# Kernel optimization log

Measured on AMD Instinct MI355X. Metric: run time of the kernel, lower is better.

The kernel has to match this reference:

```python
import jax, jax.numpy as jnp
import numpy as np

B, T, D = 4, 8192, 1024
C = 8.0


def setup_inputs() -> dict:
    key = jax.random.key(0)
    k1, k2, k3 = jax.random.split(key, 3)
    init_std = D ** (-0.5)
    x = jax.random.normal(k1, (B, T, D), dtype=jnp.float32)
    W_in = jax.random.truncated_normal(k2, -3.0, 3.0, (D, D), dtype=jnp.float32) * init_std
    W_gate = jax.random.truncated_normal(k3, -3.0, 3.0, (D, D), dtype=jnp.float32) * init_std
    b_in = jnp.zeros((D,), dtype=jnp.float32)
    b_gate = jnp.zeros((D,), dtype=jnp.float32)
    forget_lambda = jnp.linspace(-4.323, -9.0, D, dtype=jnp.float32)
    return {"x": x, "W_in": W_in, "b_in": b_in, "W_gate": W_gate,
            "b_gate": b_gate, "forget_lambda": forget_lambda}


def _combine(c1, c2):
    # linear recurrence h_t = a_t * h_{t-1} + b_t  (associative composition)
    a1, b1 = c1
    a2, b2 = c2
    return a1 * a2, a2 * b1 + b2


def reference(x, W_in, b_in, W_gate, b_gate, forget_lambda):
    # x: [B, T, D]
    input_gate = x @ W_in.T + b_in          # [B, T, D]
    recurrence_gate = x @ W_gate.T + b_gate  # [B, T, D]
    alpha = jnp.exp(-C * jax.nn.softplus(forget_lambda) * jax.nn.sigmoid(recurrence_gate))
    beta = jnp.sqrt(1.0 - alpha ** 2 + 1e-6)
    xbeta = beta * jax.nn.sigmoid(input_gate) * x
    # parallel scan of h_t = alpha_t * h_{t-1} + xbeta_t along sequence axis
    _, h = jax.lax.associative_scan(_combine, (alpha, xbeta), axis=1)
    return h
```

## Files before the change

kernel.cpp:

```cpp
#include <hip/hip_runtime.h>

typedef unsigned short u16;
typedef __attribute__((ext_vector_type(8))) short short8;
typedef __attribute__((ext_vector_type(4))) float f32x4;

#define T_SEQ 8192
#define DDIM 1024
#define BB 4
#define MM (BB * T_SEQ)
#define NC 128
#define CHUNK (T_SEQ / NC)
#define CHAINS (BB * DDIM)
#define NT 16

__device__ __forceinline__ float bf_lo(unsigned p) {
    union { unsigned u; float f; } v; v.u = p << 16; return v.f;
}
__device__ __forceinline__ float bf_hi(unsigned p) {
    union { unsigned u; float f; } v; v.u = p & 0xffff0000u; return v.f;
}
__device__ __forceinline__ float bf_u16(u16 p) {
    union { unsigned u; float f; } v; v.u = ((unsigned)p) << 16; return v.f;
}
__device__ __forceinline__ u16 f2bf(float f) {
    union { unsigned u; float f; } v; v.f = f;
    unsigned r = v.u + 0x7fffu + ((v.u >> 16) & 1u);
    return (u16)(r >> 16);
}
__device__ __forceinline__ float sigm(float z) {
    return __builtin_amdgcn_rcpf(1.0f + __expf(-z));
}
__device__ __forceinline__ void gld16(const u16* g, u16* l) {
    __builtin_amdgcn_global_load_lds((const __attribute__((address_space(1))) void*)g,
                                     (__attribute__((address_space(3))) void*)l, 16, 0, 0);
}

#define N4X (MM * DDIM / 4)
#define N4W (DDIM * DDIM / 4)
__global__ __launch_bounds__(256) void cvt_all(const float* __restrict__ x,
                                               const float* __restrict__ Wi,
                                               const float* __restrict__ Wg,
                                               u16* __restrict__ Xb,
                                               u16* __restrict__ Wib,
                                               u16* __restrict__ Wgb) {
    int i = blockIdx.x * 256 + threadIdx.x;
    const float* src; u16* dst; int j;
    if (i < N4X)            { src = x;  dst = Xb;  j = i; }
    else if (i < N4X + N4W) { src = Wi; dst = Wib; j = i - N4X; }
    else                    { src = Wg; dst = Wgb; j = i - N4X - N4W; }
    float4 v = ((const float4*)src)[j];
    ushort4 o;
    o.x = f2bf(v.x); o.y = f2bf(v.y); o.z = f2bf(v.z); o.w = f2bf(v.w);
    ((ushort4*)dst)[j] = o;
}


#define MFMA_ROW(i_, av)                                                              \
    acc[i_][0] = __builtin_amdgcn_mfma_f32_16x16x32_bf16(av, b0, acc[i_][0], 0, 0, 0); \
    acc[i_][1] = __builtin_amdgcn_mfma_f32_16x16x32_bf16(av, b1, acc[i_][1], 0, 0, 0); \
    acc[i_][2] = __builtin_amdgcn_mfma_f32_16x16x32_bf16(av, b2, acc[i_][2], 0, 0, 0); \
    acc[i_][3] = __builtin_amdgcn_mfma_f32_16x16x32_bf16(av, b3, acc[i_][3], 0, 0, 0);

#define MFMA_Q(ib) MFMA_ROW((ib)+0, a0) MFMA_ROW((ib)+1, a1) MFMA_ROW((ib)+2, a2) MFMA_ROW((ib)+3, a3)

#define PH_TAIL(IB)                                          \
    __builtin_amdgcn_s_barrier();                            \
    asm volatile("s_waitcnt lgkmcnt(0)" ::: "memory");       \
    __builtin_amdgcn_sched_barrier(0);                       \
    __builtin_amdgcn_s_setprio(1);                           \
    MFMA_Q(IB)                                               \
    __builtin_amdgcn_s_setprio(0);                           \
    __builtin_amdgcn_s_barrier();                            \
    __builtin_amdgcn_sched_barrier(0);

#define STA(buf, kh, rb, t_) gld16(gA + (size_t)(t_)*64 + (kh)*32 + (size_t)(rb)*128*DDIM, \
                                   &lds[(((buf)*2 + (kh))*1024 + (rb)*512 + tid)*8])
#define STB(buf, kh, hf, t_) gld16(((hf) ? gBg : gBi) + (size_t)(t_)*64 + (kh)*32,          \
                                   &lds[32768 + (((buf)*2 + (kh))*1024 + (hf)*512 + tid)*8])

#define LDA(kk, i) (*(const short8*)&lds[((cur*2 + (kk))*256 + arow0 + (i)*16)*32 + aoff])
#define LDB(kk, j) (*(const short8*)&lds[32768 + ((cur*2 + (kk))*256 + brow0 + (j)*16)*32 + aoff])

__global__ __launch_bounds__(512, 2)
void gemm_fused(const u16* __restrict__ X, const u16* __restrict__ Wi,
                const u16* __restrict__ Wg, const float* __restrict__ b_in,
                const float* __restrict__ b_gate, const float* __restrict__ lam,
                u16* __restrict__ Sg, u16* __restrict__ XBg) {
    const int bid = blockIdx.x;
    const int xcd = bid & 7;
    const int r = bid >> 3;
    const int n_tile = r & 7;
    const int m_tile = xcd * 16 + (r >> 3);
    const int tN0 = n_tile * 128;
    const int tM0 = m_tile * 256;

    const int tid = threadIdx.x;
    const int lane = tid & 63;
    const int w = tid >> 6;
    const int wm = w >> 2;
    const int wn = w & 3;
    const int gate = wn >> 1;
    const int wn_sub = wn & 1;

    __shared__ u16 lds[65536];

    const int srow = tid >> 2;
    const int c8log = (tid & 3) ^ ((tid >> 3) & 3);
    const u16* gA  = X  + (size_t)(tM0 + srow) * DDIM + c8log * 8;
    const u16* gBi = Wi + (size_t)(tN0 + srow) * DDIM + c8log * 8;
    const u16* gBg = Wg + (size_t)(tN0 + srow) * DDIM + c8log * 8;

    const int lm = lane & 15;
    const int aoff = (((lane >> 4) ^ ((lm >> 1) & 3))) * 8;
    const int arow0 = wm * 128 + lm;
    const int brow0 = gate * 128 + wn_sub * 64 + lm;

    f32x4 acc[8][4] = {};
    short8 a0, a1, a2, a3, b0, b1, b2, b3;

    STA(0, 0, 0, 0); STA(0, 0, 1, 0); STB(0, 0, 0, 0); STB(0, 0, 1, 0);
    STA(0, 1, 0, 0); STA(0, 1, 1, 0); STB(0, 1, 0, 0); STB(0, 1, 1, 0);
    asm volatile("s_waitcnt vmcnt(4)" ::: "memory");
    __builtin_amdgcn_s_barrier();
    __builtin_amdgcn_sched_barrier(0);

    for (int t = 0; t < NT - 1; ++t) {
        const int cur = t & 1, nb = cur ^ 1, tn = t + 1;
        b0 = LDB(0, 0); b1 = LDB(0, 1); b2 = LDB(0, 2); b3 = LDB(0, 3);
        a0 = LDA(0, 0); a1 = LDA(0, 1); a2 = LDA(0, 2); a3 = LDA(0, 3);
        STA(nb, 0, 0, tn); STA(nb, 0, 1, tn);
        PH_TAIL(0)
        a0 = LDA(0, 4); a1 = LDA(0, 5); a2 = LDA(0, 6); a3 = LDA(0, 7);
        STB(nb, 0, 0, tn); STB(nb, 0, 1, tn);
        asm volatile("s_waitcnt vmcnt(4)" ::: "memory");
        PH_TAIL(4)
        b0 = LDB(1, 0); b1 = LDB(1, 1); b2 = LDB(1, 2); b3 = LDB(1, 3);
        a0 = LDA(1, 0); a1 = LDA(1, 1); a2 = LDA(1, 2); a3 = LDA(1, 3);
        STA(nb, 1, 0, tn); STA(nb, 1, 1, tn);
        PH_TAIL(0)
        a0 = LDA(1, 4); a1 = LDA(1, 5); a2 = LDA(1, 6); a3 = LDA(1, 7);
        STB(nb, 1, 0, tn); STB(nb, 1, 1, tn);
        asm volatile("s_waitcnt vmcnt(4)" ::: "memory");
        PH_TAIL(4)
    }
    {
        const int cur = (NT - 1) & 1;
        b0 = LDB(0, 0); b1 = LDB(0, 1); b2 = LDB(0, 2); b3 = LDB(0, 3);
        a0 = LDA(0, 0); a1 = LDA(0, 1); a2 = LDA(0, 2); a3 = LDA(0, 3);
        PH_TAIL(0)
        a0 = LDA(0, 4); a1 = LDA(0, 5); a2 = LDA(0, 6); a3 = LDA(0, 7);
        asm volatile("s_waitcnt vmcnt(0)" ::: "memory");
        PH_TAIL(4)
        b0 = LDB(1, 0); b1 = LDB(1, 1); b2 = LDB(1, 2); b3 = LDB(1, 3);
        a0 = LDA(1, 0); a1 = LDA(1, 1); a2 = LDA(1, 2); a3 = LDA(1, 3);
        PH_TAIL(0)
        a0 = LDA(1, 4); a1 = LDA(1, 5); a2 = LDA(1, 6); a3 = LDA(1, 7);
        PH_TAIL(4)
    }

    const int pair = wm * 2 + wn_sub;
    const int r0 = (lane >> 4) << 2;
    const int cb = lane & 15;
    if (gate) {
#pragma unroll
        for (int j = 0; j < 4; ++j) {
            const int colg = tN0 + wn_sub * 64 + j * 16 + cb;
            const float bj = b_gate[colg];
            const float nsp = -8.0f * log1pf(__expf(lam[colg]));
#pragma unroll
            for (int i = 0; i < 8; ++i) {
                const int rowb = tM0 + wm * 128 + i * 16 + r0;
#pragma unroll
                for (int rr = 0; rr < 4; ++rr) {
                    float s = nsp * sigm(acc[i][j][rr] + bj);
                    u16 sb = f2bf(s);
                    Sg[(size_t)(rowb + rr) * DDIM + colg] = sb;
                    lds[((pair * 8 + i) * 16 + j * 4 + rr) * 64 + lane] = sb;
                }
            }
        }
    }
    asm volatile("s_waitcnt lgkmcnt(0)" ::: "memory");
    __builtin_amdgcn_s_barrier();
    __builtin_amdgcn_sched_barrier(0);
    if (!gate) {
#pragma unroll
        for (int j = 0; j < 4; ++j) {
            const int colg = tN0 + wn_sub * 64 + j * 16 + cb;
            const float bj = b_in[colg];
#pragma unroll
            for (int i = 0; i < 8; ++i) {
                const int rowb = tM0 + wm * 128 + i * 16 + r0;
#pragma unroll
                for (int rr = 0; rr < 4; ++rr) {
                    float s = bf_u16(lds[((pair * 8 + i) * 16 + j * 4 + rr) * 64 + lane]);
                    float a2v = __expf(2.0f * s);
                    float be = sqrtf(1.0f - a2v + 1e-6f);
                    float p = sigm(acc[i][j][rr] + bj);
                    float xv = bf_u16(X[(size_t)(rowb + rr) * DDIM + colg]);
                    XBg[(size_t)(rowb + rr) * DDIM + colg] = f2bf(be * p * xv);
                }
            }
        }
    }
}

__global__ __launch_bounds__(256)
void scan_pass1(const u16* __restrict__ S, const u16* __restrict__ XB,
                float* __restrict__ AggA, float* __restrict__ AggB) {
    const int c = blockIdx.x, dblk = blockIdx.y, bq = blockIdx.z;
    const int d0 = dblk * 512 + threadIdx.x * 2;
    size_t base = ((size_t)(bq * T_SEQ + c * CHUNK)) * DDIM + d0;

    float A0 = 1.0f, B0 = 0.0f, A1 = 1.0f, B1 = 0.0f;
#pragma unroll 8
    for (int t = 0; t < CHUNK; t++) {
        unsigned sp = *(const unsigned*)(S + base);
        unsigned xp = *(const unsigned*)(XB + base);
        float a0 = __expf(bf_lo(sp));
        float a1 = __expf(bf_hi(sp));
        B0 = fmaf(a0, B0, bf_lo(xp)); A0 *= a0;
        B1 = fmaf(a1, B1, bf_hi(xp)); A1 *= a1;
        base += DDIM;
    }
    const int chain = bq * DDIM + d0;
    float2 av; av.x = A0; av.y = A1;
    float2 bv; bv.x = B0; bv.y = B1;
    *(float2*)(AggA + (size_t)c * CHAINS + chain) = av;
    *(float2*)(AggB + (size_t)c * CHAINS + chain) = bv;
}

__global__ __launch_bounds__(256)
void scan_pass2(const float* __restrict__ AggA, const float* __restrict__ AggB,
                float* __restrict__ H0) {
    const int chain = blockIdx.x * 256 + threadIdx.x;
    float p = 0.0f;
#pragma unroll 8
    for (int c = 0; c < NC; c++) {
        H0[(size_t)c * CHAINS + chain] = p;
        p = AggA[(size_t)c * CHAINS + chain] * p + AggB[(size_t)c * CHAINS + chain];
    }
}

__global__ __launch_bounds__(256)
void scan_pass3(const u16* __restrict__ S, const u16* __restrict__ XB,
                const float* __restrict__ H0, float* __restrict__ out) {
    const int c = blockIdx.x, dblk = blockIdx.y, bq = blockIdx.z;
    const int d0 = dblk * 512 + threadIdx.x * 2;
    size_t base = ((size_t)(bq * T_SEQ + c * CHUNK)) * DDIM + d0;
    const int chain = bq * DDIM + d0;

    float2 h = *(const float2*)(H0 + (size_t)c * CHAINS + chain);
#pragma unroll 8
    for (int t = 0; t < CHUNK; t++) {
        unsigned sp = *(const unsigned*)(S + base);
        unsigned xp = *(const unsigned*)(XB + base);
        float a0 = __expf(bf_lo(sp));
        float a1 = __expf(bf_hi(sp));
        h.x = fmaf(a0, h.x, bf_lo(xp));
        h.y = fmaf(a1, h.y, bf_hi(xp));
        *(float2*)(out + base) = h;
        base += DDIM;
    }
}

extern "C" void kernel_launch(void* const* d_in, const int* in_sizes, int n_in,
                              void* d_out, int out_size, void* d_ws, size_t ws_size,
                              hipStream_t stream) {
    const float* x   = (const float*)d_in[0];
    const float* Win = (const float*)d_in[1];
    const float* bin = (const float*)d_in[2];
    const float* Wg  = (const float*)d_in[3];
    const float* bg  = (const float*)d_in[4];
    const float* lam = (const float*)d_in[5];
    float* out = (float*)d_out;

    char* w = (char*)d_ws;
    u16* Wi_bf  = (u16*)(w);
    u16* Wg_bf  = (u16*)(w + (size_t)(2) * 1024 * 1024);
    u16* Sg     = (u16*)(w + (size_t)(4) * 1024 * 1024);
    u16* XBg    = (u16*)(w + (size_t)(68) * 1024 * 1024);
    float* AggA = (float*)(w + (size_t)(132) * 1024 * 1024);
    float* AggB = (float*)(w + (size_t)(134) * 1024 * 1024);
    float* H0   = (float*)(w + (size_t)(136) * 1024 * 1024);

    u16* Xbf = (u16*)d_out;

    cvt_all<<<dim3((N4X + 2 * N4W) / 256), dim3(256), 0, stream>>>(
        x, Win, Wg, Xbf, Wi_bf, Wg_bf);

    gemm_fused<<<dim3((DDIM / 128) * (MM / 256)), dim3(512), 0, stream>>>(
        Xbf, Wi_bf, Wg_bf, bin, bg, lam, Sg, XBg);

    scan_pass1<<<dim3(NC, 2, BB), dim3(256), 0, stream>>>(Sg, XBg, AggA, AggB);
    scan_pass2<<<dim3(CHAINS / 256), dim3(256), 0, stream>>>(AggA, AggB, H0);
    scan_pass3<<<dim3(NC, 2, BB), dim3(256), 0, stream>>>(Sg, XBg, H0, out);
}
```

Before: 521.1 us.

## Stage gate epilogue through swizzled LDS for vectorized stores; merge MFMA phases

The GEMM epilogue now writes both the recurrence-gate term and the quantized input-gate sigmoid into XOR-swizzled LDS tiles. All threads then do 16-byte vectorized reads of X and 16-byte stores of S and XB, replacing scattered 2-byte global stores and loads. The main loop also goes from four half-phases with split LDS reads to two full phases: all A/B fragments are read, then 32 MFMAs run between barriers. This raises register pressure, and storing the sigmoid as 16-bit fixed point changes precision slightly.

Result: faster. 477.4 us (-8.4%).

```diff
diff --git a/kernel.cpp b/kernel.cpp
--- a/kernel.cpp
+++ b/kernel.cpp
@@ -55,23 +55,19 @@
 }
 
 
-#define MFMA_ROW(i_, av)                                                              \
+#define MROW(i_, av)                                                                   \
     acc[i_][0] = __builtin_amdgcn_mfma_f32_16x16x32_bf16(av, b0, acc[i_][0], 0, 0, 0); \
     acc[i_][1] = __builtin_amdgcn_mfma_f32_16x16x32_bf16(av, b1, acc[i_][1], 0, 0, 0); \
     acc[i_][2] = __builtin_amdgcn_mfma_f32_16x16x32_bf16(av, b2, acc[i_][2], 0, 0, 0); \
     acc[i_][3] = __builtin_amdgcn_mfma_f32_16x16x32_bf16(av, b3, acc[i_][3], 0, 0, 0);
 
-#define MFMA_Q(ib) MFMA_ROW((ib)+0, a0) MFMA_ROW((ib)+1, a1) MFMA_ROW((ib)+2, a2) MFMA_ROW((ib)+3, a3)
-
-#define PH_TAIL(IB)                                          \
-    __builtin_amdgcn_s_barrier();                            \
-    asm volatile("s_waitcnt lgkmcnt(0)" ::: "memory");       \
-    __builtin_amdgcn_sched_barrier(0);                       \
-    __builtin_amdgcn_s_setprio(1);                           \
-    MFMA_Q(IB)                                               \
-    __builtin_amdgcn_s_setprio(0);                           \
-    __builtin_amdgcn_s_barrier();                            \
-    __builtin_amdgcn_sched_barrier(0);
+#define MALL MROW(0, a0) MROW(1, a1) MROW(2, a2) MROW(3, a3) \
+             MROW(4, a4) MROW(5, a5) MROW(6, a6) MROW(7, a7)
+
+#define RDALL(kk)                                                            \
+    b0 = LDB(kk, 0); b1 = LDB(kk, 1); b2 = LDB(kk, 2); b3 = LDB(kk, 3);      \
+    a0 = LDA(kk, 0); a1 = LDA(kk, 1); a2 = LDA(kk, 2); a3 = LDA(kk, 3);      \
+    a4 = LDA(kk, 4); a5 = LDA(kk, 5); a6 = LDA(kk, 6); a7 = LDA(kk, 7);
 
 #define STA(buf, kh, rb, t_) gld16(gA + (size_t)(t_)*64 + (kh)*32 + (size_t)(rb)*128*DDIM, \
                                    &lds[(((buf)*2 + (kh))*1024 + (rb)*512 + tid)*8])
@@ -116,92 +112,112 @@
     const int brow0 = gate * 128 + wn_sub * 64 + lm;
 
     f32x4 acc[8][4] = {};
-    short8 a0, a1, a2, a3, b0, b1, b2, b3;
+    short8 a0, a1, a2, a3, a4, a5, a6, a7, b0, b1, b2, b3;
 
     STA(0, 0, 0, 0); STA(0, 0, 1, 0); STB(0, 0, 0, 0); STB(0, 0, 1, 0);
     STA(0, 1, 0, 0); STA(0, 1, 1, 0); STB(0, 1, 0, 0); STB(0, 1, 1, 0);
     asm volatile("s_waitcnt vmcnt(4)" ::: "memory");
     __builtin_amdgcn_s_barrier();
-    __builtin_amdgcn_sched_barrier(0);
 
     for (int t = 0; t < NT - 1; ++t) {
         const int cur = t & 1, nb = cur ^ 1, tn = t + 1;
-        b0 = LDB(0, 0); b1 = LDB(0, 1); b2 = LDB(0, 2); b3 = LDB(0, 3);
-        a0 = LDA(0, 0); a1 = LDA(0, 1); a2 = LDA(0, 2); a3 = LDA(0, 3);
-        STA(nb, 0, 0, tn); STA(nb, 0, 1, tn);
-        PH_TAIL(0)
-        a0 = LDA(0, 4); a1 = LDA(0, 5); a2 = LDA(0, 6); a3 = LDA(0, 7);
-        STB(nb, 0, 0, tn); STB(nb, 0, 1, tn);
+        RDALL(0)
+        STA(nb, 0, 0, tn); STA(nb, 0, 1, tn); STB(nb, 0, 0, tn); STB(nb, 0, 1, tn);
         asm volatile("s_waitcnt vmcnt(4)" ::: "memory");
-        PH_TAIL(4)
-        b0 = LDB(1, 0); b1 = LDB(1, 1); b2 = LDB(1, 2); b3 = LDB(1, 3);
-        a0 = LDA(1, 0); a1 = LDA(1, 1); a2 = LDA(1, 2); a3 = LDA(1, 3);
-        STA(nb, 1, 0, tn); STA(nb, 1, 1, tn);
-        PH_TAIL(0)
-        a0 = LDA(1, 4); a1 = LDA(1, 5); a2 = LDA(1, 6); a3 = LDA(1, 7);
-        STB(nb, 1, 0, tn); STB(nb, 1, 1, tn);
+        __builtin_amdgcn_s_barrier();
+        __builtin_amdgcn_s_setprio(1);
+        MALL
+        __builtin_amdgcn_s_setprio(0);
+        __builtin_amdgcn_s_barrier();
+        RDALL(1)
+        STA(nb, 1, 0, tn); STA(nb, 1, 1, tn); STB(nb, 1, 0, tn); STB(nb, 1, 1, tn);
         asm volatile("s_waitcnt vmcnt(4)" ::: "memory");
-        PH_TAIL(4)
+        __builtin_amdgcn_s_barrier();
+        __builtin_amdgcn_s_setprio(1);
+        MALL
+        __builtin_amdgcn_s_setprio(0);
+        __builtin_amdgcn_s_barrier();
     }
     {
         const int cur = (NT - 1) & 1;
-        b0 = LDB(0, 0); b1 = LDB(0, 1); b2 = LDB(0, 2); b3 = LDB(0, 3);
-        a0 = LDA(0, 0); a1 = LDA(0, 1); a2 = LDA(0, 2); a3 = LDA(0, 3);
-        PH_TAIL(0)
-        a0 = LDA(0, 4); a1 = LDA(0, 5); a2 = LDA(0, 6); a3 = LDA(0, 7);
+        RDALL(0)
         asm volatile("s_waitcnt vmcnt(0)" ::: "memory");
-        PH_TAIL(4)
-        b0 = LDB(1, 0); b1 = LDB(1, 1); b2 = LDB(1, 2); b3 = LDB(1, 3);
-        a0 = LDA(1, 0); a1 = LDA(1, 1); a2 = LDA(1, 2); a3 = LDA(1, 3);
-        PH_TAIL(0)
-        a0 = LDA(1, 4); a1 = LDA(1, 5); a2 = LDA(1, 6); a3 = LDA(1, 7);
-        PH_TAIL(4)
-    }
-
-    const int pair = wm * 2 + wn_sub;
+        __builtin_amdgcn_s_barrier();
+        __builtin_amdgcn_s_setprio(1);
+        MALL
+        __builtin_amdgcn_s_setprio(0);
+        __builtin_amdgcn_s_barrier();
+        RDALL(1)
+        __builtin_amdgcn_s_setprio(1);
+        MALL
+        __builtin_amdgcn_s_setprio(0);
+        __builtin_amdgcn_s_barrier();
+    }
+
     const int r0 = (lane >> 4) << 2;
     const int cb = lane & 15;
     if (gate) {
 #pragma unroll
         for (int j = 0; j < 4; ++j) {
             const int colg = tN0 + wn_sub * 64 + j * 16 + cb;
+            const int cl = wn_sub * 64 + j * 16 + cb;
             const float bj = b_gate[colg];
             const float nsp = -8.0f * log1pf(__expf(lam[colg]));
 #pragma unroll
             for (int i = 0; i < 8; ++i) {
-                const int rowb = tM0 + wm * 128 + i * 16 + r0;
+                const int rl0 = wm * 128 + i * 16 + r0;
 #pragma unroll
                 for (int rr = 0; rr < 4; ++rr) {
+                    const int rl = rl0 + rr;
                     float s = nsp * sigm(acc[i][j][rr] + bj);
-                    u16 sb = f2bf(s);
-                    Sg[(size_t)(rowb + rr) * DDIM + colg] = sb;
-                    lds[((pair * 8 + i) * 16 + j * 4 + rr) * 64 + lane] = sb;
+                    lds[rl * 128 + (cl ^ (((rl >> 2) & 7) << 4))] = f2bf(s);
                 }
             }
         }
+    } else {
+#pragma unroll
+        for (int j = 0; j < 4; ++j) {
+            const int colg = tN0 + wn_sub * 64 + j * 16 + cb;
+            const int cl = wn_sub * 64 + j * 16 + cb;
+            const float bj = b_in[colg];
+#pragma unroll
+            for (int i = 0; i < 8; ++i) {
+                const int rl0 = wm * 128 + i * 16 + r0;
+#pragma unroll
+                for (int rr = 0; rr < 4; ++rr) {
+                    const int rl = rl0 + rr;
+                    float p = sigm(acc[i][j][rr] + bj);
+                    lds[32768 + rl * 128 + (cl ^ (((rl >> 2) & 7) << 4))] =
+                        (u16)(p * 65535.0f + 0.5f);
+                }
+            }
+        }
     }
     asm volatile("s_waitcnt lgkmcnt(0)" ::: "memory");
     __builtin_amdgcn_s_barrier();
     __builtin_amdgcn_sched_barrier(0);
-    if (!gate) {
-#pragma unroll
-        for (int j = 0; j < 4; ++j) {
-            const int colg = tN0 + wn_sub * 64 + j * 16 + cb;
-            const float bj = b_in[colg];
-#pragma unroll
-            for (int i = 0; i < 8; ++i) {
-                const int rowb = tM0 + wm * 128 + i * 16 + r0;
-#pragma unroll
-                for (int rr = 0; rr < 4; ++rr) {
-                    float s = bf_u16(lds[((pair * 8 + i) * 16 + j * 4 + rr) * 64 + lane]);
-                    float a2v = __expf(2.0f * s);
-                    float be = sqrtf(1.0f - a2v + 1e-6f);
-                    float p = sigm(acc[i][j][rr] + bj);
-                    float xv = bf_u16(X[(size_t)(rowb + rr) * DDIM + colg]);
-                    XBg[(size_t)(rowb + rr) * DDIM + colg] = f2bf(be * p * xv);
-                }
-            }
+
+    const int cc = tid & 15;
+    const int rg0 = (tid >> 4) * 8;
+#pragma unroll
+    for (int k = 0; k < 8; ++k) {
+        const int rl = rg0 + k;
+        const int ch = (cc ^ (((rl >> 2) & 7) << 1)) * 8;
+        short8 sv = *(const short8*)&lds[rl * 128 + ch];
+        short8 pv = *(const short8*)&lds[32768 + rl * 128 + ch];
+        const size_t go = (size_t)(tM0 + rl) * DDIM + tN0 + cc * 8;
+        short8 xv = *(const short8*)&X[go];
+        short8 ov;
+#pragma unroll
+        for (int e = 0; e < 8; ++e) {
+            float s = bf_u16((u16)sv[e]);
+            float p = (float)((u16)pv[e]) * (1.0f / 65535.0f);
+            float xf = bf_u16((u16)xv[e]);
+            float be = sqrtf(1.0f - __expf(2.0f * s) + 1e-6f);
+            ov[e] = (short)f2bf(be * p * xf);
         }
+        *(short8*)&Sg[go] = sv;
+        *(short8*)&XBg[go] = ov;
     }
 }
 
```
